# Optimization experiments

Measured on AMD Instinct MI355X. Metric: run time of the kernel, lower is better.

## Reference

```python
import jax, jax.numpy as jnp
import numpy as np

SEQ_LEN = 64  # config.SEQ_LEN
T, B, N, D = 256, 128, 4, 2
H_HIS, H_INT = 32, 8


def _uniform(key, shape, k):
    return jax.random.uniform(key, shape, jnp.float32, -k, k)


def setup_inputs() -> dict:
    key = jax.random.key(0)
    ks = jax.random.split(key, 12)
    kh = 1.0 / np.sqrt(H_HIS)
    ki = 1.0 / np.sqrt(H_INT)
    ko = 1.0 / np.sqrt(40)
    return {
        "inputs": jax.random.normal(ks[0], (T, B, N, D), jnp.float32),
        # history LSTM (input 2 -> hidden 32), gate order i,f,g,o like torch
        "Wih_his": _uniform(ks[1], (4 * H_HIS, D), kh),
        "Whh_his": _uniform(ks[2], (4 * H_HIS, H_HIS), kh),
        "bih_his": _uniform(ks[3], (4 * H_HIS,), kh),
        "bhh_his": _uniform(ks[4], (4 * H_HIS,), kh),
        # interaction LSTM (input 2 -> hidden 8)
        "Wih_int": _uniform(ks[5], (4 * H_INT, D), ki),
        "Whh_int": _uniform(ks[6], (4 * H_INT, H_INT), ki),
        "bih_int": _uniform(ks[7], (4 * H_INT,), ki),
        "bhh_int": _uniform(ks[8], (4 * H_INT,), ki),
        # output Linear(40 -> 2)
        "W_out": _uniform(ks[9], (2, H_HIS + H_INT), ko),
        "b_out": _uniform(ks[10], (2,), ko),
    }


def _lstm_windows(x_w, valid, Wih, Whh, bih, bhh):
    """Run an LSTM over L steps for T independent windows at once.
    x_w: [L, Tw, B, d]  inputs per step (leading padding for short windows)
    valid: [L, Tw] bool; while False the state is held at zero, which is
    exactly equivalent to starting the window fresh at its first valid step.
    Returns final hidden state h: [Tw, B, H].
    """
    H = Whh.shape[1]
    Tw, Bb = x_w.shape[1], x_w.shape[2]
    b = bih + bhh

    def step(carry, xs):
        h, c = carry
        x, v = xs
        g = x @ Wih.T + h @ Whh.T + b            # [Tw, B, 4H]
        i, f, gg, o = jnp.split(g, 4, axis=-1)
        c_new = jax.nn.sigmoid(f) * c + jax.nn.sigmoid(i) * jnp.tanh(gg)
        h_new = jax.nn.sigmoid(o) * jnp.tanh(c_new)
        m = v[:, None, None]
        return (jnp.where(m, h_new, 0.0), jnp.where(m, c_new, 0.0)), None

    init = (jnp.zeros((Tw, Bb, H), x_w.dtype), jnp.zeros((Tw, Bb, H), x_w.dtype))
    (h, _), _ = jax.lax.scan(step, init, (x_w, valid))
    return h


def reference(inputs, Wih_his, Whh_his, bih_his, bhh_his,
              Wih_int, Whh_int, bih_int, bhh_int, W_out, b_out):
    Tt, Bb, Nn, Dd = inputs.shape
    L = SEQ_LEN
    # window index for output frame t: frames t-L+1 .. t (clipped; invalid masked)
    t = jnp.arange(Tt)[:, None]
    s = jnp.arange(L)[None, :]
    idx = t - (L - 1) + s                      # [T, L]
    valid = (idx >= 0)
    idx_c = jnp.clip(idx, 0, Tt - 1)
    x_his = inputs[:, :, -1, :][idx_c]         # [T, L, B, d] (ego / last node)
    x_int = inputs[:, :, 0, :][idx_c]          # [T, L, B, d] (interaction node)
    x_his = jnp.transpose(x_his, (1, 0, 2, 3))  # [L, T, B, d]
    x_int = jnp.transpose(x_int, (1, 0, 2, 3))
    v = jnp.transpose(valid)                   # [L, T]

    h_his = _lstm_windows(x_his, v, Wih_his, Whh_his, bih_his, bhh_his)  # [T,B,32]
    h_int = _lstm_windows(x_int, v, Wih_int, Whh_int, bih_int, bhh_int)  # [T,B,8]
    emb = jnp.concatenate([h_his, h_int], axis=-1)                       # [T,B,40]
    return emb @ W_out.T + b_out                                         # [T,B,2]
```

## Files before the change

kernel.cpp:

```cpp
#include <hip/hip_runtime.h>


typedef float v4f __attribute__((ext_vector_type(4)));
typedef _Float16 h8v __attribute__((ext_vector_type(8)));

static __device__ __forceinline__ float fexp2(float x) {
    return __builtin_amdgcn_exp2f(x);
}
static __device__ __forceinline__ float frcp(float x) {
    return __builtin_amdgcn_rcpf(x);
}
static __device__ __forceinline__ unsigned short f2h(float f) {
    _Float16 h = (_Float16)f;
    unsigned short u;
    __builtin_memcpy(&u, &h, 2);
    return u;
}
static __device__ __forceinline__ float h2f(unsigned short u) {
    _Float16 h;
    __builtin_memcpy(&h, &u, 2);
    return (float)h;
}

#define LOG2E    1.442695041f
#define TWOLOG2E 2.885390082f
#define H16ONE   0x3C00u

static __device__ __forceinline__ void lstm_unit(
    float Di, float Df, float Dg, float Do, float& c, float& h)
{
    const float ei = fminf(fexp2(Di), 1e12f);
    const float ef = fminf(fexp2(Df), 1e12f);
    const float eg = fminf(fexp2(Dg), 1e12f);
    const float eo = fminf(fexp2(Do), 1e18f);
    const float pi1 = 1.f + ei, pf1 = 1.f + ef, pg1 = 1.f + eg;
    const float p12 = pi1 * pg1;
    const float r3  = frcp(p12 * pf1);
    const float cn  = fmaf(p12, c, (1.f - eg) * pf1) * r3;
    c = cn;
    const float ec = fminf(fexp2(TWOLOG2E * cn), 1e18f);
    h = (ec - 1.f) * frcp((1.f + eo) * (1.f + ec));
}

__global__ __launch_bounds__(256) void prep_kernel(
    const float* __restrict__ Wih_his, const float* __restrict__ Whh_his,
    const float* __restrict__ bih_his, const float* __restrict__ bhh_his,
    const float* __restrict__ Wih_int, const float* __restrict__ Whh_int,
    const float* __restrict__ bih_int, const float* __restrict__ bhh_int,
    float* __restrict__ ws)
{
    const int i = blockIdx.x * 256 + threadIdx.x;
    unsigned short* wsu = reinterpret_cast<unsigned short*>(ws);

    if (i < 4096) {
        const int T8 = i >> 9, m = (i >> 5) & 15, k = i & 31;
        const int w = T8 >> 2, Tl = T8 & 3;
        const int orig = Tl * 32 + w * 16 + m;
        const float s = (Tl == 2) ? -TWOLOG2E : -LOG2E;
        wsu[i] = f2h(Whh_his[orig * 32 + k] * s);
    } else if (i < 8192) {
        const int e = i - 4096;
        const int T8 = e >> 9, m = (e >> 5) & 15, k = e & 31;
        const int w = T8 >> 2, Tl = T8 & 3;
        const int orig = Tl * 32 + w * 16 + m;
        const float s = (Tl == 2) ? -TWOLOG2E : -LOG2E;
        const float w0 = Wih_his[orig * 2] * s;
        const float w1 = Wih_his[orig * 2 + 1] * s;
        const float b  = (bih_his[orig] + bhh_his[orig]) * s;
        unsigned short v = 0;
        switch (k) {
            case 0: v = f2h(w0); break;
            case 1: v = f2h(w1); break;
            case 2: v = f2h(b);  break;
            case 3: v = f2h(w0 - h2f(f2h(w0))); break;
            case 4: v = f2h(w1 - h2f(f2h(w1))); break;
            case 5: v = f2h(b  - h2f(f2h(b)));  break;
            case 6: v = f2h(w0); break;
            case 7: v = f2h(w1); break;
            default: v = 0; break;
        }
        wsu[4096 + e] = v;
    } else if (i < 9216) {
        const int e = i - 8192;
        const int T = e >> 9, m = (e >> 5) & 15, k = e & 31;
        const int q = k >> 3, j = k & 7;
        const int g = 2 * T + ((m & 3) >> 1);
        const int u = 2 * (m >> 2) + (m & 1);
        const int orig = g * 8 + u;
        const float s = (g == 2) ? -TWOLOG2E : -LOG2E;
        unsigned short v = 0;
        if (j < 6) {
            const int col = 2 * q + (j & 1);
            const float w = Whh_int[orig * 8 + col] * s;
            v = (j == 2 || j == 3) ? f2h(w - h2f(f2h(w))) : f2h(w);
        } else {
            const int comp = j & 1;
            if (q <= 1) {
                v = f2h(Wih_int[orig * 2 + comp] * s);
            } else if (q == 2) {
                const float w = Wih_int[orig * 2 + comp] * s;
                v = f2h(w - h2f(f2h(w)));
            } else {
                const float b = (bih_int[orig] + bhh_int[orig]) * s;
                v = (comp == 0) ? f2h(b) : f2h(b - h2f(f2h(b)));
            }
        }
        wsu[8192 + e] = v;
    }
}

__global__ __launch_bounds__(128, 4) void fused2_kernel(
    const float* __restrict__ inp, const float* __restrict__ ws,
    const float* __restrict__ W_out, const float* __restrict__ b_out,
    float* __restrict__ out)
{
    __shared__ __align__(16) unsigned char hb[2][1280];
    __shared__ float2 ebuf[2][16];

    const int tid  = threadIdx.x;
    const int w    = tid >> 6;
    const int lane = tid & 63;
    const int n    = lane & 15;
    const int q    = lane >> 4;
    const int Wd   = blockIdx.x;
    const int j    = Wd >> 3;
    const int bg   = Wd & 7;
    const int tau0 = j;
    const bool readout = (j == 0);

    const unsigned short* wsu = reinterpret_cast<const unsigned short*>(ws);
    const h8v* wa = reinterpret_cast<const h8v*>(wsu);
    const h8v* wx = reinterpret_cast<const h8v*>(wsu + 4096);
    const h8v* wi = reinterpret_cast<const h8v*>(wsu + 8192);
    h8v AW[4], AX[4], AI[2];
#pragma unroll
    for (int Tl = 0; Tl < 4; ++Tl) {
        AW[Tl] = wa[(w * 4 + Tl) * 64 + n * 4 + q];
        AX[Tl] = wx[(w * 4 + Tl) * 64 + n * 4 + q];
    }
#pragma unroll
    for (int T = 0; T < 2; ++T) AI[T] = wi[T * 64 + n * 4 + q];

    const int chain = bg * 16 + n;
    const float* xb0 = inp + chain * 8;
    float2 xvH = *reinterpret_cast<const float2*>(xb0 + tau0 * 1024 + 6);
    float2 xvI = *reinterpret_cast<const float2*>(xb0 + tau0 * 1024);

    union BU { unsigned u[4]; h8v h; };
    BU bh;  bh.u[0] = bh.u[1] = bh.u[2] = bh.u[3] = 0;
    BU bhI; bhI.u[0] = bhI.u[1] = bhI.u[2] = bhI.u[3] = 0;
    float cH[4] = {0.f, 0.f, 0.f, 0.f};
    float hH[4] = {0.f, 0.f, 0.f, 0.f};
    float cI0 = 0.f, cI1 = 0.f, ih0 = 0.f, ih1 = 0.f;

    const int wb = n * 80 + w * 32 + q * 8;
    const int rb = n * 80 + q * 16;

#pragma unroll 1
    for (int s = 0; s < 64; ++s) {
        const int sn = (s < 63) ? (s + 1) : 63;
        const float* xr = xb0 + (tau0 + sn) * 1024;
        const float2 xnH = *reinterpret_cast<const float2*>(xr + 6);
        const float2 xnI = *reinterpret_cast<const float2*>(xr);

        BU bx;
        {
            const unsigned short xh = f2h(xvH.x), yh = f2h(xvH.y);
            const unsigned short xl = f2h(xvH.x - h2f(xh));
            const unsigned short yl = f2h(xvH.y - h2f(yh));
            bx.u[0] = ((unsigned)yh << 16) | xh;
            bx.u[1] = ((unsigned)xh << 16) | H16ONE;
            bx.u[2] = (H16ONE << 16) | yh;
            bx.u[3] = ((unsigned)yl << 16) | xl;
            if (q != 0) { bx.u[0] = 0; bx.u[1] = 0; bx.u[2] = 0; bx.u[3] = 0; }
        }

        const v4f z = {0.f, 0.f, 0.f, 0.f};

        if (w == 1) {
            const unsigned short xh = f2h(xvI.x), yh = f2h(xvI.y);
            const unsigned short xl = f2h(xvI.x - h2f(xh));
            const unsigned short yl = f2h(xvI.y - h2f(yh));
            const unsigned ph = ((unsigned)yh << 16) | xh;
            const unsigned pl = ((unsigned)yl << 16) | xl;
            bhI.u[3] = (q == 3) ? ((H16ONE << 16) | H16ONE)
                                : ((q == 1) ? pl : ph);
            const v4f E0 = __builtin_amdgcn_mfma_f32_16x16x32_f16(AI[0], bhI.h, z, 0, 0, 0);
            const v4f E1 = __builtin_amdgcn_mfma_f32_16x16x32_f16(AI[1], bhI.h, z, 0, 0, 0);
            lstm_unit(E0[0], E0[2], E1[0], E1[2], cI0, ih0);
            lstm_unit(E0[1], E0[3], E1[1], E1[3], cI1, ih1);
            const unsigned short hh0 = f2h(ih0), hh1 = f2h(ih1);
            const unsigned short hl0 = f2h(ih0 - h2f(hh0));
            const unsigned short hl1 = f2h(ih1 - h2f(hh1));
            bhI.u[0] = ((unsigned)hh1 << 16) | hh0;
            bhI.u[1] = bhI.u[0];
            bhI.u[2] = ((unsigned)hl1 << 16) | hl0;
        }

        v4f D[4];
#pragma unroll
        for (int Tl = 0; Tl < 4; ++Tl) {
            const v4f cx = __builtin_amdgcn_mfma_f32_16x16x32_f16(AX[Tl], bx.h, z, 0, 0, 0);
            D[Tl] = __builtin_amdgcn_mfma_f32_16x16x32_f16(AW[Tl], bh.h, cx, 0, 0, 0);
        }

#pragma unroll
        for (int r = 0; r < 4; ++r)
            lstm_unit(D[0][r], D[1][r], D[2][r], D[3][r], cH[r], hH[r]);

        float re0 = 0.f, re1 = 0.f;
        if (readout) {
            const int u0 = w * 16 + q * 4;
#pragma unroll
            for (int r = 0; r < 4; ++r) {
                re0 = fmaf(W_out[u0 + r],      hH[r], re0);
                re1 = fmaf(W_out[40 + u0 + r], hH[r], re1);
            }
            if (w == 1) {
                re0 = fmaf(W_out[33 + 2 * q], ih1, fmaf(W_out[32 + 2 * q], ih0, re0));
                re1 = fmaf(W_out[73 + 2 * q], ih1, fmaf(W_out[72 + 2 * q], ih0, re1));
            }
            re0 += __shfl_xor(re0, 16); re1 += __shfl_xor(re1, 16);
            re0 += __shfl_xor(re0, 32); re1 += __shfl_xor(re1, 32);
            if (w == 1 && lane < 16) {
                float2 p; p.x = re0; p.y = re1;
                ebuf[s & 1][n] = p;
            }
        }

        {
            const unsigned p0 = ((unsigned)f2h(hH[1]) << 16) | f2h(hH[0]);
            const unsigned p1 = ((unsigned)f2h(hH[3]) << 16) | f2h(hH[2]);
            *reinterpret_cast<uint2*>(&hb[s & 1][wb]) = make_uint2(p0, p1);
        }
        __syncthreads();
        {
            const uint4 rv = *reinterpret_cast<const uint4*>(&hb[s & 1][rb]);
            bh.u[0] = rv.x; bh.u[1] = rv.y; bh.u[2] = rv.z; bh.u[3] = rv.w;
        }

        if (readout && w == 0 && lane < 16) {
            const float2 p = ebuf[s & 1][n];
            float2 o;
            o.x = re0 + p.x + b_out[0];
            o.y = re1 + p.y + b_out[1];
            reinterpret_cast<float2*>(out)[s * 128 + chain] = o;
        }

        xvH = xnH;
        xvI = xnI;
    }

    if (!readout) {
        const int u0 = w * 16 + q * 4;
        float e0 = 0.f, e1 = 0.f;
#pragma unroll
        for (int r = 0; r < 4; ++r) {
            e0 = fmaf(W_out[u0 + r],      hH[r], e0);
            e1 = fmaf(W_out[40 + u0 + r], hH[r], e1);
        }
        if (w == 1) {
            e0 = fmaf(W_out[33 + 2 * q], ih1, fmaf(W_out[32 + 2 * q], ih0, e0));
            e1 = fmaf(W_out[73 + 2 * q], ih1, fmaf(W_out[72 + 2 * q], ih0, e1));
        }
        e0 += __shfl_xor(e0, 16); e1 += __shfl_xor(e1, 16);
        e0 += __shfl_xor(e0, 32); e1 += __shfl_xor(e1, 32);

        if (w == 1 && lane < 16) {
            float2 p; p.x = e0; p.y = e1;
            ebuf[0][n] = p;
        }
        __syncthreads();
        if (w == 0 && lane < 16) {
            const float2 p = ebuf[0][n];
            float2 o;
            o.x = e0 + p.x + b_out[0];
            o.y = e1 + p.y + b_out[1];
            reinterpret_cast<float2*>(out)[(63 + j) * 128 + chain] = o;
        }
    }
}

extern "C" void kernel_launch(void* const* d_in, const int* in_sizes, int n_in,
                              void* d_out, int out_size, void* d_ws, size_t ws_size,
                              hipStream_t stream) {
    const float* inp     = (const float*)d_in[0];
    const float* Wih_his = (const float*)d_in[1];
    const float* Whh_his = (const float*)d_in[2];
    const float* bih_his = (const float*)d_in[3];
    const float* bhh_his = (const float*)d_in[4];
    const float* Wih_int = (const float*)d_in[5];
    const float* Whh_int = (const float*)d_in[6];
    const float* bih_int = (const float*)d_in[7];
    const float* bhh_int = (const float*)d_in[8];
    const float* W_out   = (const float*)d_in[9];
    const float* b_out   = (const float*)d_in[10];
    float* out  = (float*)d_out;
    float* ws   = (float*)d_ws;

    prep_kernel<<<dim3(36), dim3(256), 0, stream>>>(
        Wih_his, Whh_his, bih_his, bhh_his,
        Wih_int, Whh_int, bih_int, bhh_int, ws);

    fused2_kernel<<<dim3(1544), dim3(128), 0, stream>>>(
        inp, ws, W_out, b_out, out);
}
```

Measured before the change: 179.4 us.

## Process two window groups per block and spread interaction LSTM across both waves

Each block now runs two independent window/batch groups (A and B) through the history LSTM, interleaving their MFMA chains so the latency of one hides the other, and halves the grid. The interaction LSTM for group A runs on wave 0 and for group B on wave 1, so both waves stay busy instead of only wave 1. This doubles per-thread register state and drops the occupancy hint in launch bounds. It also runs one barrier per step for two chains.

```diff
diff --git a/kernel.cpp b/kernel.cpp
--- a/kernel.cpp
+++ b/kernel.cpp
@@ -40,6 +40,17 @@
     c = cn;
     const float ec = fminf(fexp2(TWOLOG2E * cn), 1e18f);
     h = (ec - 1.f) * frcp((1.f + eo) * (1.f + ec));
+}
+
+static __device__ __forceinline__ void his_partial(
+    const float* __restrict__ W_out, const float hH[4], int u0,
+    float& e0, float& e1)
+{
+#pragma unroll
+    for (int r = 0; r < 4; ++r) {
+        e0 = fmaf(W_out[u0 + r],      hH[r], e0);
+        e1 = fmaf(W_out[40 + u0 + r], hH[r], e1);
+    }
 }
 
 __global__ __launch_bounds__(256) void prep_kernel(
@@ -109,24 +120,24 @@
     }
 }
 
-__global__ __launch_bounds__(128, 4) void fused2_kernel(
+__global__ __launch_bounds__(128) void fusedq_kernel(
     const float* __restrict__ inp, const float* __restrict__ ws,
     const float* __restrict__ W_out, const float* __restrict__ b_out,
     float* __restrict__ out)
 {
-    __shared__ __align__(16) unsigned char hb[2][1280];
-    __shared__ float2 ebuf[2][16];
+    __shared__ __align__(16) unsigned char hb[2][2][1280];
+    __shared__ __align__(8) float2 ebuf[2][16];
 
     const int tid  = threadIdx.x;
     const int w    = tid >> 6;
     const int lane = tid & 63;
     const int n    = lane & 15;
     const int q    = lane >> 4;
-    const int Wd   = blockIdx.x;
-    const int j    = Wd >> 3;
-    const int bg   = Wd & 7;
-    const int tau0 = j;
-    const bool readout = (j == 0);
+    const int b    = blockIdx.x;
+    const int jA   = b >> 3,        bgA = b & 7;
+    const int idB  = b + 772;
+    const int jB   = idB >> 3,      bgB = idB & 7;
+    const bool readout = (jA == 0);
 
     const unsigned short* wsu = reinterpret_cast<const unsigned short*>(ws);
     const h8v* wa = reinterpret_cast<const h8v*>(wsu);
@@ -141,16 +152,22 @@
 #pragma unroll
     for (int T = 0; T < 2; ++T) AI[T] = wi[T * 64 + n * 4 + q];
 
-    const int chain = bg * 16 + n;
-    const float* xb0 = inp + chain * 8;
-    float2 xvH = *reinterpret_cast<const float2*>(xb0 + tau0 * 1024 + 6);
-    float2 xvI = *reinterpret_cast<const float2*>(xb0 + tau0 * 1024);
+    const int chainA = bgA * 16 + n;
+    const int chainB = bgB * 16 + n;
+    const float* xbA = inp + chainA * 8;
+    const float* xbB = inp + chainB * 8;
+    float2 xvHA = *reinterpret_cast<const float2*>(xbA + jA * 1024 + 6);
+    float2 xvHB = *reinterpret_cast<const float2*>(xbB + jB * 1024 + 6);
+    const float* xbI = (w == 0) ? xbA : xbB;
+    const int    jI  = (w == 0) ? jA  : jB;
+    float2 xvI = *reinterpret_cast<const float2*>(xbI + jI * 1024);
 
     union BU { unsigned u[4]; h8v h; };
-    BU bh;  bh.u[0] = bh.u[1] = bh.u[2] = bh.u[3] = 0;
+    BU bhA; bhA.u[0] = bhA.u[1] = bhA.u[2] = bhA.u[3] = 0;
+    BU bhB; bhB.u[0] = bhB.u[1] = bhB.u[2] = bhB.u[3] = 0;
     BU bhI; bhI.u[0] = bhI.u[1] = bhI.u[2] = bhI.u[3] = 0;
-    float cH[4] = {0.f, 0.f, 0.f, 0.f};
-    float hH[4] = {0.f, 0.f, 0.f, 0.f};
+    float cHA[4] = {0.f, 0.f, 0.f, 0.f}, hHA[4] = {0.f, 0.f, 0.f, 0.f};
+    float cHB[4] = {0.f, 0.f, 0.f, 0.f}, hHB[4] = {0.f, 0.f, 0.f, 0.f};
     float cI0 = 0.f, cI1 = 0.f, ih0 = 0.f, ih1 = 0.f;
 
     const int wb = n * 80 + w * 32 + q * 8;
@@ -159,25 +176,32 @@
 #pragma unroll 1
     for (int s = 0; s < 64; ++s) {
         const int sn = (s < 63) ? (s + 1) : 63;
-        const float* xr = xb0 + (tau0 + sn) * 1024;
-        const float2 xnH = *reinterpret_cast<const float2*>(xr + 6);
-        const float2 xnI = *reinterpret_cast<const float2*>(xr);
-
-        BU bx;
-        {
-            const unsigned short xh = f2h(xvH.x), yh = f2h(xvH.y);
-            const unsigned short xl = f2h(xvH.x - h2f(xh));
-            const unsigned short yl = f2h(xvH.y - h2f(yh));
-            bx.u[0] = ((unsigned)yh << 16) | xh;
-            bx.u[1] = ((unsigned)xh << 16) | H16ONE;
-            bx.u[2] = (H16ONE << 16) | yh;
-            bx.u[3] = ((unsigned)yl << 16) | xl;
-            if (q != 0) { bx.u[0] = 0; bx.u[1] = 0; bx.u[2] = 0; bx.u[3] = 0; }
-        }
-
-        const v4f z = {0.f, 0.f, 0.f, 0.f};
-
-        if (w == 1) {
+        const float2 xnHA = *reinterpret_cast<const float2*>(xbA + (jA + sn) * 1024 + 6);
+        const float2 xnHB = *reinterpret_cast<const float2*>(xbB + (jB + sn) * 1024 + 6);
+        const float2 xnI  = *reinterpret_cast<const float2*>(xbI + (jI + sn) * 1024);
+
+        BU bxA, bxB;
+        {
+            const unsigned short xh = f2h(xvHA.x), yh = f2h(xvHA.y);
+            const unsigned short xl = f2h(xvHA.x - h2f(xh));
+            const unsigned short yl = f2h(xvHA.y - h2f(yh));
+            bxA.u[0] = ((unsigned)yh << 16) | xh;
+            bxA.u[1] = ((unsigned)xh << 16) | H16ONE;
+            bxA.u[2] = (H16ONE << 16) | yh;
+            bxA.u[3] = ((unsigned)yl << 16) | xl;
+            if (q != 0) { bxA.u[0] = 0; bxA.u[1] = 0; bxA.u[2] = 0; bxA.u[3] = 0; }
+        }
+        {
+            const unsigned short xh = f2h(xvHB.x), yh = f2h(xvHB.y);
+            const unsigned short xl = f2h(xvHB.x - h2f(xh));
+            const unsigned short yl = f2h(xvHB.y - h2f(yh));
+            bxB.u[0] = ((unsigned)yh << 16) | xh;
+            bxB.u[1] = ((unsigned)xh << 16) | H16ONE;
+            bxB.u[2] = (H16ONE << 16) | yh;
+            bxB.u[3] = ((unsigned)yl << 16) | xl;
+            if (q != 0) { bxB.u[0] = 0; bxB.u[1] = 0; bxB.u[2] = 0; bxB.u[3] = 0; }
+        }
+        {
             const unsigned short xh = f2h(xvI.x), yh = f2h(xvI.y);
             const unsigned short xl = f2h(xvI.x - h2f(xh));
             const unsigned short yl = f2h(xvI.y - h2f(yh));
@@ -185,10 +209,28 @@
             const unsigned pl = ((unsigned)yl << 16) | xl;
             bhI.u[3] = (q == 3) ? ((H16ONE << 16) | H16ONE)
                                 : ((q == 1) ? pl : ph);
-            const v4f E0 = __builtin_amdgcn_mfma_f32_16x16x32_f16(AI[0], bhI.h, z, 0, 0, 0);
-            const v4f E1 = __builtin_amdgcn_mfma_f32_16x16x32_f16(AI[1], bhI.h, z, 0, 0, 0);
-            lstm_unit(E0[0], E0[2], E1[0], E1[2], cI0, ih0);
-            lstm_unit(E0[1], E0[3], E1[1], E1[3], cI1, ih1);
+        }
+
+        const v4f z = {0.f, 0.f, 0.f, 0.f};
+
+        const v4f E0 = __builtin_amdgcn_mfma_f32_16x16x32_f16(AI[0], bhI.h, z, 0, 0, 0);
+        const v4f E1 = __builtin_amdgcn_mfma_f32_16x16x32_f16(AI[1], bhI.h, z, 0, 0, 0);
+
+        v4f DA[4], DB[4];
+#pragma unroll
+        for (int Tl = 0; Tl < 4; ++Tl) {
+            const v4f cx = __builtin_amdgcn_mfma_f32_16x16x32_f16(AX[Tl], bxA.h, z, 0, 0, 0);
+            DA[Tl] = __builtin_amdgcn_mfma_f32_16x16x32_f16(AW[Tl], bhA.h, cx, 0, 0, 0);
+        }
+#pragma unroll
+        for (int Tl = 0; Tl < 4; ++Tl) {
+            const v4f cx = __builtin_amdgcn_mfma_f32_16x16x32_f16(AX[Tl], bxB.h, z, 0, 0, 0);
+            DB[Tl] = __builtin_amdgcn_mfma_f32_16x16x32_f16(AW[Tl], bhB.h, cx, 0, 0, 0);
+        }
+
+        lstm_unit(E0[0], E0[2], E1[0], E1[2], cI0, ih0);
+        lstm_unit(E0[1], E0[3], E1[1], E1[3], cI1, ih1);
+        {
             const unsigned short hh0 = f2h(ih0), hh1 = f2h(ih1);
             const unsigned short hl0 = f2h(ih0 - h2f(hh0));
             const unsigned short hl1 = f2h(ih1 - h2f(hh1));
@@ -197,29 +239,30 @@
             bhI.u[2] = ((unsigned)hl1 << 16) | hl0;
         }
 
-        v4f D[4];
-#pragma unroll
-        for (int Tl = 0; Tl < 4; ++Tl) {
-            const v4f cx = __builtin_amdgcn_mfma_f32_16x16x32_f16(AX[Tl], bx.h, z, 0, 0, 0);
-            D[Tl] = __builtin_amdgcn_mfma_f32_16x16x32_f16(AW[Tl], bh.h, cx, 0, 0, 0);
-        }
-
 #pragma unroll
         for (int r = 0; r < 4; ++r)
-            lstm_unit(D[0][r], D[1][r], D[2][r], D[3][r], cH[r], hH[r]);
+            lstm_unit(DA[0][r], DA[1][r], DA[2][r], DA[3][r], cHA[r], hHA[r]);
+        {
+            const unsigned p0 = ((unsigned)f2h(hHA[1]) << 16) | f2h(hHA[0]);
+            const unsigned p1 = ((unsigned)f2h(hHA[3]) << 16) | f2h(hHA[2]);
+            *reinterpret_cast<uint2*>(&hb[s & 1][0][wb]) = make_uint2(p0, p1);
+        }
+#pragma unroll
+        for (int r = 0; r < 4; ++r)
+            lstm_unit(DB[0][r], DB[1][r], DB[2][r], DB[3][r], cHB[r], hHB[r]);
+        {
+            const unsigned p0 = ((unsigned)f2h(hHB[1]) << 16) | f2h(hHB[0]);
+            const unsigned p1 = ((unsigned)f2h(hHB[3]) << 16) | f2h(hHB[2]);
+            *reinterpret_cast<uint2*>(&hb[s & 1][1][wb]) = make_uint2(p0, p1);
+        }
 
         float re0 = 0.f, re1 = 0.f;
         if (readout) {
-            const int u0 = w * 16 + q * 4;
-#pragma unroll
-            for (int r = 0; r < 4; ++r) {
-                re0 = fmaf(W_out[u0 + r],      hH[r], re0);
-                re1 = fmaf(W_out[40 + u0 + r], hH[r], re1);
+            if (w == 0) {
+                re0 = fmaf(W_out[33 + 2 * q], ih1, W_out[32 + 2 * q] * ih0);
+                re1 = fmaf(W_out[73 + 2 * q], ih1, W_out[72 + 2 * q] * ih0);
             }
-            if (w == 1) {
-                re0 = fmaf(W_out[33 + 2 * q], ih1, fmaf(W_out[32 + 2 * q], ih0, re0));
-                re1 = fmaf(W_out[73 + 2 * q], ih1, fmaf(W_out[72 + 2 * q], ih0, re1));
-            }
+            his_partial(W_out, hHA, w * 16 + q * 4, re0, re1);
             re0 += __shfl_xor(re0, 16); re1 += __shfl_xor(re1, 16);
             re0 += __shfl_xor(re0, 32); re1 += __shfl_xor(re1, 32);
             if (w == 1 && lane < 16) {
@@ -228,15 +271,13 @@
             }
         }
 
-        {
-            const unsigned p0 = ((unsigned)f2h(hH[1]) << 16) | f2h(hH[0]);
-            const unsigned p1 = ((unsigned)f2h(hH[3]) << 16) | f2h(hH[2]);
-            *reinterpret_cast<uint2*>(&hb[s & 1][wb]) = make_uint2(p0, p1);
-        }
         __syncthreads();
-        {
-            const uint4 rv = *reinterpret_cast<const uint4*>(&hb[s & 1][rb]);
-            bh.u[0] = rv.x; bh.u[1] = rv.y; bh.u[2] = rv.z; bh.u[3] = rv.w;
+
+        {
+            const uint4 rA = *reinterpret_cast<const uint4*>(&hb[s & 1][0][rb]);
+            bhA.u[0] = rA.x; bhA.u[1] = rA.y; bhA.u[2] = rA.z; bhA.u[3] = rA.w;
+            const uint4 rB = *reinterpret_cast<const uint4*>(&hb[s & 1][1][rb]);
+            bhB.u[0] = rB.x; bhB.u[1] = rB.y; bhB.u[2] = rB.z; bhB.u[3] = rB.w;
         }
 
         if (readout && w == 0 && lane < 16) {
@@ -244,40 +285,49 @@
             float2 o;
             o.x = re0 + p.x + b_out[0];
             o.y = re1 + p.y + b_out[1];
-            reinterpret_cast<float2*>(out)[s * 128 + chain] = o;
-        }
-
-        xvH = xnH;
-        xvI = xnI;
-    }
-
-    if (!readout) {
-        const int u0 = w * 16 + q * 4;
-        float e0 = 0.f, e1 = 0.f;
-#pragma unroll
-        for (int r = 0; r < 4; ++r) {
-            e0 = fmaf(W_out[u0 + r],      hH[r], e0);
-            e1 = fmaf(W_out[40 + u0 + r], hH[r], e1);
-        }
-        if (w == 1) {
-            e0 = fmaf(W_out[33 + 2 * q], ih1, fmaf(W_out[32 + 2 * q], ih0, e0));
-            e1 = fmaf(W_out[73 + 2 * q], ih1, fmaf(W_out[72 + 2 * q], ih0, e1));
-        }
-        e0 += __shfl_xor(e0, 16); e1 += __shfl_xor(e1, 16);
-        e0 += __shfl_xor(e0, 32); e1 += __shfl_xor(e1, 32);
-
-        if (w == 1 && lane < 16) {
-            float2 p; p.x = e0; p.y = e1;
-            ebuf[0][n] = p;
-        }
-        __syncthreads();
-        if (w == 0 && lane < 16) {
+            reinterpret_cast<float2*>(out)[s * 128 + chainA] = o;
+        }
+
+        xvHA = xnHA; xvHB = xnHB; xvI = xnI;
+    }
+
+    __syncthreads();
+
+    float eA0 = 0.f, eA1 = 0.f, eB0 = 0.f, eB1 = 0.f;
+    if (w == 0) {
+        eA0 = fmaf(W_out[33 + 2 * q], ih1, W_out[32 + 2 * q] * ih0);
+        eA1 = fmaf(W_out[73 + 2 * q], ih1, W_out[72 + 2 * q] * ih0);
+    } else {
+        eB0 = fmaf(W_out[33 + 2 * q], ih1, W_out[32 + 2 * q] * ih0);
+        eB1 = fmaf(W_out[73 + 2 * q], ih1, W_out[72 + 2 * q] * ih0);
+    }
+    his_partial(W_out, hHA, w * 16 + q * 4, eA0, eA1);
+    his_partial(W_out, hHB, w * 16 + q * 4, eB0, eB1);
+    eA0 += __shfl_xor(eA0, 16); eA1 += __shfl_xor(eA1, 16);
+    eA0 += __shfl_xor(eA0, 32); eA1 += __shfl_xor(eA1, 32);
+    eB0 += __shfl_xor(eB0, 16); eB1 += __shfl_xor(eB1, 16);
+    eB0 += __shfl_xor(eB0, 32); eB1 += __shfl_xor(eB1, 32);
+
+    if (w == 1 && lane < 16) {
+        float2 pa; pa.x = eA0; pa.y = eA1;
+        float2 pb; pb.x = eB0; pb.y = eB1;
+        ebuf[0][n] = pa;
+        ebuf[1][n] = pb;
+    }
+    __syncthreads();
+    if (w == 0 && lane < 16) {
+        if (!readout) {
             const float2 p = ebuf[0][n];
             float2 o;
-            o.x = e0 + p.x + b_out[0];
-            o.y = e1 + p.y + b_out[1];
-            reinterpret_cast<float2*>(out)[(63 + j) * 128 + chain] = o;
-        }
+            o.x = eA0 + p.x + b_out[0];
+            o.y = eA1 + p.y + b_out[1];
+            reinterpret_cast<float2*>(out)[(63 + jA) * 128 + chainA] = o;
+        }
+        const float2 p = ebuf[1][n];
+        float2 o;
+        o.x = eB0 + p.x + b_out[0];
+        o.y = eB1 + p.y + b_out[1];
+        reinterpret_cast<float2*>(out)[(63 + jB) * 128 + chainB] = o;
     }
 }
 
@@ -302,6 +352,6 @@
         Wih_his, Whh_his, bih_his, bhh_his,
         Wih_int, Whh_int, bih_int, bhh_int, ws);
 
-    fused2_kernel<<<dim3(1544), dim3(128), 0, stream>>>(
+    fusedq_kernel<<<dim3(772), dim3(128), 0, stream>>>(
         inp, ws, W_out, b_out, out);
 }
```

Result: slower. 188.4 us (+5.0%).
